# Optimization experiments

Measured on AMD Instinct MI355X. Metric: run time of the kernel, lower is better.

Reference implementation:

```python
import jax, jax.numpy as jnp
import numpy as np

C_IN = 64      # in_channels
C_OUT = 64     # out_channels
LOC = 2        # locality_size
K = 2 * LOC + 1   # kernel size = 5
B, H, W = 4, 128, 128


def _init_lateral_weights():
    # Matches LateralLayer._init_lateral_weights: 1 at (co, co*K*K + LOC*K + LOC)
    w = np.zeros((C_OUT, C_IN * K * K), np.float32)
    for co in range(C_OUT):
        cii = co * K * K + LOC * K + LOC  # center tap of matching input channel
        w[co, cii] = 1.0
    return jnp.asarray(w).reshape(C_OUT, C_IN * K * K, 1, 1)


def setup_inputs() -> dict:
    key = jax.random.key(0)
    # binary input (the layer asserts x in {0,1})
    x = jax.random.bernoulli(key, 0.1, (B, C_IN, H, W)).astype(jnp.float32)
    return {"x": x, "W_lateral": _init_lateral_weights()}


def _rearrange(x):
    # Faithful to F.conv2d(x, W_rearrange, padding='same') with the one-hot
    # indicator kernel: out[b, i*K*K + j*K + kk, h, w] = x_pad[b, i, h+j, w+kk].
    # Implemented as an unfold via K*K shifted slices (same math, no O((CKK)^2) conv).
    p = LOC
    xp = jnp.pad(x, ((0, 0), (0, 0), (p, p), (p, p)))
    Hh, Ww = x.shape[2], x.shape[3]
    patches = [xp[:, :, j:j + Hh, kk:kk + Ww] for j in range(K) for kk in range(K)]
    xr = jnp.stack(patches, axis=2)              # (B, C, K*K, H, W)
    return xr.reshape(x.shape[0], x.shape[1] * K * K, Hh, Ww)


def reference(x, W_lateral):
    xr = _rearrange(x)                                  # (B, C*K*K, H, W)
    w = W_lateral.reshape(W_lateral.shape[0], -1)       # (O, C*K*K)
    # 1x1 conv == channel contraction
    x_lateral = jnp.einsum('bkhw,ok->bohw', xr, w)      # (B, O, H, W)
    # conv with ones_like(W_lateral) == channel sum, same for every out channel
    x_max_act = jnp.sum(xr, axis=1, keepdims=True)      # (B, 1, H, W)
    min_support = float(K)
    x_max_act = jnp.maximum(x_max_act, min_support)
    xn = x_lateral / x_max_act
    xn = xn / (1e-10 + jnp.sum(w, axis=1)[None, :, None, None])
    xn = xn / (1e-10 + jnp.max(xn, axis=(2, 3), keepdims=True))
    # ts == 0 -> no temporal averaging with x_lateral_norm_prev
    x_lateral_bin = (xn ** 3 >= 0.5).astype(jnp.float32)
    return x_lateral, xn, x_lateral_bin
```

## Files before the change

### kernel.cpp

```cpp
#include <hip/hip_runtime.h>

constexpr int Bb  = 4;
constexpr int C   = 64;
constexpr int H   = 128;
constexpr int Wd  = 128;
constexpr int K   = 5;
constexpr int LOC = 2;
constexpr int KK  = K * K;
constexpr int CKK = C * KK;
constexpr int HW  = H * Wd;
constexpr int N   = Bb * C * HW;

typedef float v4f __attribute__((ext_vector_type(4)));

__device__ __forceinline__ float frcp(float x) { return __builtin_amdgcn_rcpf(x); }
__device__ __forceinline__ void nt_store4(float* p, v4f v) {
    __builtin_nontemporal_store(v, reinterpret_cast<v4f*>(p));
}

__global__ void __launch_bounds__(256) k_prep(const float* __restrict__ x,
                                              float* __restrict__ M) {
    __shared__ float S[6][Wd];
    const int t = threadIdx.x;
    const int b = blockIdx.x >> 6;
    const int strip = blockIdx.x & 63;
    const int r0 = strip * 2;

    if (t < 192) {
        const int lr = t >> 5;
        const int c0 = (t & 31) * 4;
        const int gr = r0 - 2 + lr;
        v4f s = {0.f, 0.f, 0.f, 0.f};
        if ((unsigned)gr < (unsigned)H) {
            const float* p = x + (((size_t)b * C) * H + gr) * Wd + c0;
#pragma unroll
            for (int c = 0; c < C; ++c) {
                const v4f v = *reinterpret_cast<const v4f*>(p + (size_t)c * HW);
                s += v;
            }
        }
        *reinterpret_cast<v4f*>(&S[lr][c0]) = s;
    }
    __syncthreads();

    const int lr = t >> 7;
    const int w  = t & 127;
    const int gr = r0 + lr;
    float s = 0.f;
#pragma unroll
    for (int j = 0; j < K; ++j) {
        const float* row = S[lr + j];
#pragma unroll
        for (int kk = 0; kk < K; ++kk) {
            const int ww = w + kk - LOC;
            if ((unsigned)ww < (unsigned)Wd) s += row[ww];
        }
    }
    M[b * HW + gr * Wd + w] = fmaxf(s, (float)K);
}

__global__ void __launch_bounds__(1024) k_main(
    const float* __restrict__ x, const float* __restrict__ wgt,
    const float* __restrict__ M, float* __restrict__ out0,
    float* __restrict__ out1, float* __restrict__ out2) {
    __shared__ int   s_k[CKK];
    __shared__ float s_v[CKK];
    __shared__ int   s_cnt;
    __shared__ float s_wsum;
    __shared__ float s_red[16];
    __shared__ float s_rinv;

    const int tid = threadIdx.x;
    const int plane = blockIdx.x;
    const int o = plane & (C - 1);
    const int b = plane >> 6;

    if (tid == 0) { s_cnt = 0; s_wsum = 0.0f; }
    __syncthreads();

    const float* wrow = wgt + o * CKK;
    for (int k = tid; k < CKK; k += 1024) {
        float v = wrow[k];
        if (v != 0.0f) {
            int pos = atomicAdd(&s_cnt, 1);
            s_k[pos] = k;
            s_v[pos] = v;
            atomicAdd(&s_wsum, v);
        }
    }
    __syncthreads();
    const int   n   = s_cnt;
    const float rws = frcp(1e-10f + s_wsum);

    const float* xb = x + (size_t)b * C * HW;
    float* o0 = out0 + (size_t)plane * HW;
    float* o1 = out1 + (size_t)plane * HW;
    float* o2 = out2 + (size_t)plane * HW;
    const float* Mb = M + b * HW;

    v4f t[4];
    float lmax = -INFINITY;
#pragma unroll
    for (int it = 0; it < 4; ++it) {
        const int p = it * 4096 + tid * 4;
        const int h = p >> 7, w = p & 127;
        v4f acc = {0.f, 0.f, 0.f, 0.f};
        for (int e = 0; e < n; ++e) {
            const int   k = s_k[e];
            const float v = s_v[e];
            const int c  = k / KK;
            const int r  = k - c * KK;
            const int rj = r / K;
            const int dj = rj - LOC;
            const int dk = (r - rj * K) - LOC;
            const int hh = h + dj;
            if ((unsigned)hh < (unsigned)H) {
                const float* rowp = xb + c * HW + hh * Wd;
                const int wb = w + dk;
                float x0 = ((unsigned)(wb + 0) < (unsigned)Wd) ? rowp[wb + 0] : 0.f;
                float x1 = ((unsigned)(wb + 1) < (unsigned)Wd) ? rowp[wb + 1] : 0.f;
                float x2 = ((unsigned)(wb + 2) < (unsigned)Wd) ? rowp[wb + 2] : 0.f;
                float x3 = ((unsigned)(wb + 3) < (unsigned)Wd) ? rowp[wb + 3] : 0.f;
                acc.x += v * x0; acc.y += v * x1; acc.z += v * x2; acc.w += v * x3;
            }
        }
        nt_store4(o0 + p, acc);
        const v4f Mv = *reinterpret_cast<const v4f*>(Mb + p);
        v4f tv;
        tv.x = acc.x * frcp(Mv.x) * rws;
        tv.y = acc.y * frcp(Mv.y) * rws;
        tv.z = acc.z * frcp(Mv.z) * rws;
        tv.w = acc.w * frcp(Mv.w) * rws;
        t[it] = tv;
        lmax = fmaxf(lmax, fmaxf(fmaxf(tv.x, tv.y), fmaxf(tv.z, tv.w)));
    }

#pragma unroll
    for (int m = 32; m > 0; m >>= 1) lmax = fmaxf(lmax, __shfl_xor(lmax, m, 64));
    if ((tid & 63) == 0) s_red[tid >> 6] = lmax;
    __syncthreads();
    if (tid == 0) {
        float r = s_red[0];
#pragma unroll
        for (int q = 1; q < 16; ++q) r = fmaxf(r, s_red[q]);
        s_rinv = frcp(1e-10f + r);
    }
    __syncthreads();
    const float rinv = s_rinv;

#pragma unroll
    for (int it = 0; it < 4; ++it) {
        const int p = it * 4096 + tid * 4;
        const v4f tv = t[it];
        v4f xn, bn;
        xn = tv * rinv;
        bn.x = (xn.x * xn.x * xn.x >= 0.5f) ? 1.f : 0.f;
        bn.y = (xn.y * xn.y * xn.y >= 0.5f) ? 1.f : 0.f;
        bn.z = (xn.z * xn.z * xn.z >= 0.5f) ? 1.f : 0.f;
        bn.w = (xn.w * xn.w * xn.w >= 0.5f) ? 1.f : 0.f;
        nt_store4(o1 + p, xn);
        nt_store4(o2 + p, bn);
    }
}

extern "C" void kernel_launch(void* const* d_in, const int* in_sizes, int n_in,
                              void* d_out, int out_size, void* d_ws, size_t ws_size,
                              hipStream_t stream) {
    const float* x   = (const float*)d_in[0];
    const float* wgt = (const float*)d_in[1];
    float* out = (float*)d_out;
    float* M   = (float*)d_ws;

    float* out0 = out;
    float* out1 = out + N;
    float* out2 = out + 2 * N;

    k_prep<<<Bb * 64, 256, 0, stream>>>(x, M);
    k_main<<<Bb * C, 1024, 0, stream>>>(x, wgt, M, out0, out1, out2);
}
```

Baseline: 92.46 us.

## Fuse prep and main kernels via cooperative launch with grid sync

Merges the channel-sum/box-filter prep kernel into the main kernel and launches a single cooperative kernel of 256 blocks of 1024 threads. Each block computes its strip of the support map M, then a grid-wide barrier ensures M is complete before the per-plane lateral pass. This removes one kernel launch and the gap between kernels. In exchange it adds the grid sync cost and cooperative launch overhead, and it requires all 256 blocks to be co-resident.

```diff
diff --git a/kernel.cpp b/kernel.cpp
--- a/kernel.cpp
+++ b/kernel.cpp
@@ -1,4 +1,7 @@
 #include <hip/hip_runtime.h>
+#include <hip/hip_cooperative_groups.h>
+
+namespace cg = cooperative_groups;
 
 constexpr int Bb  = 4;
 constexpr int C   = 64;
@@ -18,55 +21,15 @@
     __builtin_nontemporal_store(v, reinterpret_cast<v4f*>(p));
 }
 
-__global__ void __launch_bounds__(256) k_prep(const float* __restrict__ x,
-                                              float* __restrict__ M) {
-    __shared__ float S[6][Wd];
-    const int t = threadIdx.x;
-    const int b = blockIdx.x >> 6;
-    const int strip = blockIdx.x & 63;
-    const int r0 = strip * 2;
-
-    if (t < 192) {
-        const int lr = t >> 5;
-        const int c0 = (t & 31) * 4;
-        const int gr = r0 - 2 + lr;
-        v4f s = {0.f, 0.f, 0.f, 0.f};
-        if ((unsigned)gr < (unsigned)H) {
-            const float* p = x + (((size_t)b * C) * H + gr) * Wd + c0;
-#pragma unroll
-            for (int c = 0; c < C; ++c) {
-                const v4f v = *reinterpret_cast<const v4f*>(p + (size_t)c * HW);
-                s += v;
-            }
-        }
-        *reinterpret_cast<v4f*>(&S[lr][c0]) = s;
-    }
-    __syncthreads();
-
-    const int lr = t >> 7;
-    const int w  = t & 127;
-    const int gr = r0 + lr;
-    float s = 0.f;
-#pragma unroll
-    for (int j = 0; j < K; ++j) {
-        const float* row = S[lr + j];
-#pragma unroll
-        for (int kk = 0; kk < K; ++kk) {
-            const int ww = w + kk - LOC;
-            if ((unsigned)ww < (unsigned)Wd) s += row[ww];
-        }
-    }
-    M[b * HW + gr * Wd + w] = fmaxf(s, (float)K);
-}
-
-__global__ void __launch_bounds__(1024) k_main(
+__global__ void __launch_bounds__(1024, 1) k_fused(
     const float* __restrict__ x, const float* __restrict__ wgt,
-    const float* __restrict__ M, float* __restrict__ out0,
+    float* __restrict__ M, float* __restrict__ out0,
     float* __restrict__ out1, float* __restrict__ out2) {
     __shared__ int   s_k[CKK];
     __shared__ float s_v[CKK];
     __shared__ int   s_cnt;
     __shared__ float s_wsum;
+    __shared__ float S[6][Wd];
     __shared__ float s_red[16];
     __shared__ float s_rinv;
 
@@ -88,7 +51,43 @@
             atomicAdd(&s_wsum, v);
         }
     }
+
+    const int bb    = blockIdx.x >> 6;
+    const int strip = blockIdx.x & 63;
+    const int r0 = strip * 2;
+    if (tid < 192) {
+        const int lr = tid >> 5;
+        const int c0 = (tid & 31) * 4;
+        const int gr = r0 - 2 + lr;
+        v4f s = {0.f, 0.f, 0.f, 0.f};
+        if ((unsigned)gr < (unsigned)H) {
+            const float* p = x + (((size_t)bb * C) * H + gr) * Wd + c0;
+#pragma unroll
+            for (int c = 0; c < C; ++c)
+                s += *reinterpret_cast<const v4f*>(p + (size_t)c * HW);
+        }
+        *reinterpret_cast<v4f*>(&S[lr][c0]) = s;
+    }
     __syncthreads();
+    if (tid < 256) {
+        const int lr = tid >> 7;
+        const int w  = tid & 127;
+        const int gr = r0 + lr;
+        float s = 0.f;
+#pragma unroll
+        for (int j = 0; j < K; ++j) {
+            const float* row = S[lr + j];
+#pragma unroll
+            for (int kk = 0; kk < K; ++kk) {
+                const int ww = w + kk - LOC;
+                if ((unsigned)ww < (unsigned)Wd) s += row[ww];
+            }
+        }
+        M[bb * HW + gr * Wd + w] = fmaxf(s, (float)K);
+    }
+
+    cg::this_grid().sync();
+
     const int   n   = s_cnt;
     const float rws = frcp(1e-10f + s_wsum);
 
@@ -175,6 +174,8 @@
     float* out1 = out + N;
     float* out2 = out + 2 * N;
 
-    k_prep<<<Bb * 64, 256, 0, stream>>>(x, M);
-    k_main<<<Bb * C, 1024, 0, stream>>>(x, wgt, M, out0, out1, out2);
+    void* args[] = {(void*)&x, (void*)&wgt, (void*)&M,
+                    (void*)&out0, (void*)&out1, (void*)&out2};
+    hipLaunchCooperativeKernel((const void*)k_fused, dim3(Bb * C), dim3(1024),
+                               args, 0, stream);
 }
```

After: 126.3 us. 1.37x slower.
